# Optimization experiments

Measured on AMD Instinct MI355X. Metric: run time of the kernel, lower is better.

## Reference

```python
import jax, jax.numpy as jnp
import numpy as np

NUM_HEADS = 32      # query heads
NUM_KV_HEADS = 8    # GQA kv heads
HEAD_DIM = 128
BS = 16             # decode batch (one new token per sequence)
KV_LEN = 2048       # pages (page_size=1 -> tokens) per sequence
NUM_SLOTS = BS * KV_LEN
SCALE = HEAD_DIM ** -0.5


def setup_inputs() -> dict:
    key = jax.random.key(0)
    ks = jax.random.split(key, 6)
    q = jax.random.normal(ks[0], (BS, NUM_HEADS * HEAD_DIM), dtype=jnp.float32)
    k = jax.random.normal(ks[1], (BS, NUM_KV_HEADS * HEAD_DIM), dtype=jnp.float32)
    v = jax.random.normal(ks[2], (BS, NUM_KV_HEADS * HEAD_DIM), dtype=jnp.float32)
    k_cache = jax.random.normal(ks[3], (NUM_SLOTS, NUM_KV_HEADS * HEAD_DIM), dtype=jnp.float32)
    v_cache = jax.random.normal(ks[4], (NUM_SLOTS, NUM_KV_HEADS * HEAD_DIM), dtype=jnp.float32)
    # paged layout: each sequence owns KV_LEN non-contiguous slots (page_size=1)
    perm = jax.random.permutation(ks[5], NUM_SLOTS).astype(jnp.int32)
    page_indices = perm.reshape(BS, KV_LEN)            # [BS, KV_LEN] slot ids
    slot_mapping = page_indices[:, -1]                 # new token written to last page
    return {"q": q, "k": k, "v": v, "k_cache": k_cache, "v_cache": v_cache,
            "slot_mapping": slot_mapping, "page_indices": page_indices}


def reference(q, k, v, k_cache, v_cache, slot_mapping, page_indices):
    # store_kvcache: scatter new K/V rows into flat [num_slots, Hkv*d] caches
    k_cache = k_cache.at[slot_mapping].set(k)
    v_cache = v_cache.at[slot_mapping].set(v)
    # paged gather (page_size=1): [BS, KV_LEN, Hkv, d]
    keys = k_cache[page_indices].reshape(BS, KV_LEN, NUM_KV_HEADS, HEAD_DIM)
    vals = v_cache[page_indices].reshape(BS, KV_LEN, NUM_KV_HEADS, HEAD_DIM)
    # GQA: query head h uses kv head h // group
    group = NUM_HEADS // NUM_KV_HEADS
    qh = q.reshape(BS, NUM_KV_HEADS, group, HEAD_DIM)
    scores = jnp.einsum('bhgd,blhd->bhgl', qh, keys) * SCALE   # [BS,Hkv,g,L]
    p = jax.nn.softmax(scores, axis=-1)
    o = jnp.einsum('bhgl,blhd->bhgd', p, vals)                 # [BS,Hkv,g,d]
    return o.reshape(BS, NUM_HEADS * HEAD_DIM)
```

## Files before the change

### kernel.cpp

```cpp
#include <hip/hip_runtime.h>
#include <math.h>

constexpr int NUM_HEADS    = 32;
constexpr int NUM_KV_HEADS = 8;
constexpr int HEAD_DIM     = 128;
constexpr int BS           = 16;
constexpr int KV_LEN       = 2048;
constexpr int GROUP        = NUM_HEADS / NUM_KV_HEADS;
constexpr int NCHUNK       = 16;
constexpr int CHUNK        = KV_LEN / NCHUNK;
constexpr int NIT          = CHUNK / 16;

__global__ __launch_bounds__(256, 4) void attn_partial_kernel(
    const float* __restrict__ q,
    const float* __restrict__ knew,
    const float* __restrict__ vnew,
    const float* __restrict__ k_cache,
    const float* __restrict__ v_cache,
    const int*   __restrict__ page_indices,
    float* __restrict__ ws_o,
    float* __restrict__ ws_m,
    float* __restrict__ ws_s)
{
    const int bid   = blockIdx.x;
    const int chunk = bid % NCHUNK;
    const int h     = (bid / NCHUNK) % NUM_KV_HEADS;
    const int b     = bid / (NCHUNK * NUM_KV_HEADS);

    const int tid  = threadIdx.x;
    const int wid  = tid >> 6;
    const int lane = tid & 63;
    const int g    = lane >> 4;
    const int sub  = lane & 15;
    const int lg   = wid * 4 + g;

    const int lbase = chunk * CHUNK;

    const float qscale = 0.08838834764831845f * 1.4426950408889634f;

    float qv[GROUP][8];
#pragma unroll
    for (int hg = 0; hg < GROUP; ++hg) {
        const float* qp = q + ((size_t)b * NUM_HEADS + h * GROUP + hg) * HEAD_DIM;
        const float4 a = *(const float4*)(qp + sub * 4);
        const float4 c = *(const float4*)(qp + 64 + sub * 4);
        qv[hg][0] = a.x * qscale; qv[hg][1] = a.y * qscale;
        qv[hg][2] = a.z * qscale; qv[hg][3] = a.w * qscale;
        qv[hg][4] = c.x * qscale; qv[hg][5] = c.y * qscale;
        qv[hg][6] = c.z * qscale; qv[hg][7] = c.w * qscale;
    }

    float m[GROUP], ssum[GROUP], o[GROUP][8];
#pragma unroll
    for (int hg = 0; hg < GROUP; ++hg) {
        m[hg] = -INFINITY; ssum[hg] = 0.f;
#pragma unroll
        for (int j = 0; j < 8; ++j) o[hg][j] = 0.f;
    }

    const float* knew_row = knew + ((size_t)b * NUM_KV_HEADS + h) * HEAD_DIM;
    const float* vnew_row = vnew + ((size_t)b * NUM_KV_HEADS + h) * HEAD_DIM;

    int idx_next = page_indices[b * KV_LEN + lbase + lg];

#pragma unroll 1
    for (int it = 0; it < NIT; ++it) {
        const int l   = lbase + it * 16 + lg;
        const int idx = idx_next;
        if (it + 1 < NIT)
            idx_next = page_indices[b * KV_LEN + l + 16];

        const float* kr;
        const float* vr;
        if (l == KV_LEN - 1) {
            kr = knew_row; vr = vnew_row;
        } else {
            kr = k_cache + ((size_t)idx * NUM_KV_HEADS + h) * HEAD_DIM;
            vr = v_cache + ((size_t)idx * NUM_KV_HEADS + h) * HEAD_DIM;
        }
        const float4 k0 = *(const float4*)(kr + sub * 4);
        const float4 k1 = *(const float4*)(kr + 64 + sub * 4);
        const float4 v0 = *(const float4*)(vr + sub * 4);
        const float4 v1 = *(const float4*)(vr + 64 + sub * 4);

        float sc[GROUP];
#pragma unroll
        for (int hg = 0; hg < GROUP; ++hg) {
            sc[hg] = qv[hg][0] * k0.x + qv[hg][1] * k0.y + qv[hg][2] * k0.z + qv[hg][3] * k0.w
                   + qv[hg][4] * k1.x + qv[hg][5] * k1.y + qv[hg][6] * k1.z + qv[hg][7] * k1.w;
        }
#pragma unroll
        for (int off = 1; off < 16; off <<= 1) {
#pragma unroll
            for (int hg = 0; hg < GROUP; ++hg)
                sc[hg] += __shfl_xor(sc[hg], off, 64);
        }
#pragma unroll
        for (int hg = 0; hg < GROUP; ++hg) {
            const float mn = fmaxf(m[hg], sc[hg]);
            const float cf = exp2f(m[hg] - mn);
            const float pr = exp2f(sc[hg] - mn);
            ssum[hg] = ssum[hg] * cf + pr;
            m[hg] = mn;
            o[hg][0] = o[hg][0] * cf + pr * v0.x;
            o[hg][1] = o[hg][1] * cf + pr * v0.y;
            o[hg][2] = o[hg][2] * cf + pr * v0.z;
            o[hg][3] = o[hg][3] * cf + pr * v0.w;
            o[hg][4] = o[hg][4] * cf + pr * v1.x;
            o[hg][5] = o[hg][5] * cf + pr * v1.y;
            o[hg][6] = o[hg][6] * cf + pr * v1.z;
            o[hg][7] = o[hg][7] * cf + pr * v1.w;
        }
    }

#pragma unroll
    for (int off = 16; off <= 32; off <<= 1) {
#pragma unroll
        for (int hg = 0; hg < GROUP; ++hg) {
            const float mo = __shfl_xor(m[hg], off, 64);
            const float so = __shfl_xor(ssum[hg], off, 64);
            float oo[8];
#pragma unroll
            for (int j = 0; j < 8; ++j) oo[j] = __shfl_xor(o[hg][j], off, 64);
            const float mn = fmaxf(m[hg], mo);
            const float c1 = exp2f(m[hg] - mn);
            const float c2 = exp2f(mo - mn);
            ssum[hg] = ssum[hg] * c1 + so * c2;
#pragma unroll
            for (int j = 0; j < 8; ++j) o[hg][j] = o[hg][j] * c1 + oo[j] * c2;
            m[hg] = mn;
        }
    }

    __shared__ float red_o[4][GROUP][HEAD_DIM];
    __shared__ float red_m[4][GROUP];
    __shared__ float red_s[4][GROUP];
    if (lane < 16) {
#pragma unroll
        for (int hg = 0; hg < GROUP; ++hg) {
            *(float4*)&red_o[wid][hg][sub * 4]      = make_float4(o[hg][0], o[hg][1], o[hg][2], o[hg][3]);
            *(float4*)&red_o[wid][hg][64 + sub * 4] = make_float4(o[hg][4], o[hg][5], o[hg][6], o[hg][7]);
        }
        if (sub == 0) {
#pragma unroll
            for (int hg = 0; hg < GROUP; ++hg) { red_m[wid][hg] = m[hg]; red_s[wid][hg] = ssum[hg]; }
        }
    }
    __syncthreads();

    if (wid == 0) {
        const int hg = g;
        const float mn = fmaxf(fmaxf(red_m[0][hg], red_m[1][hg]),
                               fmaxf(red_m[2][hg], red_m[3][hg]));
        float stot = 0.f;
        float acc[8] = {0.f,0.f,0.f,0.f,0.f,0.f,0.f,0.f};
#pragma unroll
        for (int w = 0; w < 4; ++w) {
            const float c = exp2f(red_m[w][hg] - mn);
            stot += red_s[w][hg] * c;
#pragma unroll
            for (int j = 0; j < 4; ++j) acc[j]     += red_o[w][hg][sub * 4 + j] * c;
#pragma unroll
            for (int j = 0; j < 4; ++j) acc[4 + j] += red_o[w][hg][64 + sub * 4 + j] * c;
        }
        const size_t pbase = (((size_t)chunk * BS + b) * NUM_KV_HEADS + h) * GROUP + hg;
        float* op = ws_o + pbase * HEAD_DIM;
        *(float4*)(op + sub * 4)      = make_float4(acc[0], acc[1], acc[2], acc[3]);
        *(float4*)(op + 64 + sub * 4) = make_float4(acc[4], acc[5], acc[6], acc[7]);
        if (sub == 0) { ws_m[pbase] = mn; ws_s[pbase] = stot; }
    }
}

__global__ __launch_bounds__(128) void attn_combine_kernel(
    const float* __restrict__ ws_o,
    const float* __restrict__ ws_m,
    const float* __restrict__ ws_s,
    float* __restrict__ out)
{
    const int bid = blockIdx.x;
    const int hg  = bid % GROUP;
    const int h   = (bid / GROUP) % NUM_KV_HEADS;
    const int b   = bid / (GROUP * NUM_KV_HEADS);
    const int d   = threadIdx.x;

    float mv[NCHUNK];
    float mx = -INFINITY;
#pragma unroll
    for (int c = 0; c < NCHUNK; ++c) {
        mv[c] = ws_m[(((size_t)c * BS + b) * NUM_KV_HEADS + h) * GROUP + hg];
        mx = fmaxf(mx, mv[c]);
    }
    float stot = 0.f, acc = 0.f;
#pragma unroll
    for (int c = 0; c < NCHUNK; ++c) {
        const size_t pbase = (((size_t)c * BS + b) * NUM_KV_HEADS + h) * GROUP + hg;
        const float cf = exp2f(mv[c] - mx);
        stot += ws_s[pbase] * cf;
        acc  += ws_o[pbase * HEAD_DIM + d] * cf;
    }
    out[((size_t)b * NUM_HEADS + h * GROUP + hg) * HEAD_DIM + d] = acc / stot;
}

extern "C" void kernel_launch(void* const* d_in, const int* in_sizes, int n_in,
                              void* d_out, int out_size, void* d_ws, size_t ws_size,
                              hipStream_t stream)
{
    const float* q       = (const float*)d_in[0];
    const float* k       = (const float*)d_in[1];
    const float* v       = (const float*)d_in[2];
    const float* k_cache = (const float*)d_in[3];
    const float* v_cache = (const float*)d_in[4];
    const int* page_indices = (const int*)d_in[6];
    float* out = (float*)d_out;

    float* ws_o = (float*)d_ws;
    float* ws_m = ws_o + (size_t)NCHUNK * BS * NUM_KV_HEADS * GROUP * HEAD_DIM;
    float* ws_s = ws_m + (size_t)NCHUNK * BS * NUM_KV_HEADS * GROUP;

    attn_partial_kernel<<<BS * NUM_KV_HEADS * NCHUNK, 256, 0, stream>>>(
        q, k, v, k_cache, v_cache, page_indices, ws_o, ws_m, ws_s);
    attn_combine_kernel<<<BS * NUM_KV_HEADS * GROUP, 128, 0, stream>>>(
        ws_o, ws_m, ws_s, out);
}
```

Before: 53.72 us.

## Double-buffer paged K/V rows into LDS via async global_load_lds

Each wave now uses global_load_lds DMA to copy its 16 gathered K/V rows into a double-buffered shared-memory region. The next iteration's rows are issued before the current one is consumed from LDS, so the scattered page loads can overlap with the dot-product and softmax work. The reduction scratch now reuses the same shared buffer. In exchange, every iteration needs a block-wide barrier, and correctness depends on the compiler inserting the right wait counts for the async LDS writes.

After: 58.30 us. 1.09x slower.

```diff
diff --git a/kernel.cpp b/kernel.cpp
--- a/kernel.cpp
+++ b/kernel.cpp
@@ -10,6 +10,13 @@
 constexpr int NCHUNK       = 16;
 constexpr int CHUNK        = KV_LEN / NCHUNK;
 constexpr int NIT          = CHUNK / 16;
+
+__device__ __forceinline__ void dma16(const float* g, float* l) {
+    __builtin_amdgcn_global_load_lds(
+        (const __attribute__((address_space(1))) void*)g,
+        (__attribute__((address_space(3))) void*)l,
+        16, 0, 0);
+}
 
 __global__ __launch_bounds__(256, 4) void attn_partial_kernel(
     const float* __restrict__ q,
@@ -36,6 +43,8 @@
 
     const int lbase = chunk * CHUNK;
 
+    __shared__ float smem[2][4][1024];
+
     const float qscale = 0.08838834764831845f * 1.4426950408889634f;
 
     float qv[GROUP][8];
@@ -61,27 +70,40 @@
     const float* knew_row = knew + ((size_t)b * NUM_KV_HEADS + h) * HEAD_DIM;
     const float* vnew_row = vnew + ((size_t)b * NUM_KV_HEADS + h) * HEAD_DIM;
 
-    int idx_next = page_indices[b * KV_LEN + lbase + lg];
-
-#pragma unroll 1
-    for (int it = 0; it < NIT; ++it) {
-        const int l   = lbase + it * 16 + lg;
-        const int idx = idx_next;
-        if (it + 1 < NIT)
-            idx_next = page_indices[b * KV_LEN + l + 16];
-
-        const float* kr;
-        const float* vr;
+    auto stage = [&](int buf, int l, int idx) {
+        const float *kr, *vr;
         if (l == KV_LEN - 1) {
             kr = knew_row; vr = vnew_row;
         } else {
             kr = k_cache + ((size_t)idx * NUM_KV_HEADS + h) * HEAD_DIM;
             vr = v_cache + ((size_t)idx * NUM_KV_HEADS + h) * HEAD_DIM;
         }
-        const float4 k0 = *(const float4*)(kr + sub * 4);
-        const float4 k1 = *(const float4*)(kr + 64 + sub * 4);
-        const float4 v0 = *(const float4*)(vr + sub * 4);
-        const float4 v1 = *(const float4*)(vr + 64 + sub * 4);
+        float* base = &smem[buf][wid][0];
+        dma16(kr + sub * 4,       base);
+        dma16(kr + 64 + sub * 4,  base + 256);
+        dma16(vr + sub * 4,       base + 512);
+        dma16(vr + 64 + sub * 4,  base + 768);
+    };
+
+    int idx_cur = page_indices[b * KV_LEN + lbase + lg];
+    stage(0, lbase + lg, idx_cur);
+    int idx_next = page_indices[b * KV_LEN + lbase + ((NIT > 1) ? 16 : 0) + lg];
+
+#pragma unroll 1
+    for (int t = 0; t < NIT; ++t) {
+        __syncthreads();
+
+        if (t + 1 < NIT) {
+            stage((t + 1) & 1, lbase + (t + 1) * 16 + lg, idx_next);
+            if (t + 2 < NIT)
+                idx_next = page_indices[b * KV_LEN + lbase + (t + 2) * 16 + lg];
+        }
+
+        const float* basep = &smem[t & 1][wid][0];
+        const float4 k0 = *(const float4*)(basep + g * 64 + sub * 4);
+        const float4 k1 = *(const float4*)(basep + 256 + g * 64 + sub * 4);
+        const float4 v0 = *(const float4*)(basep + 512 + g * 64 + sub * 4);
+        const float4 v1 = *(const float4*)(basep + 768 + g * 64 + sub * 4);
 
         float sc[GROUP];
 #pragma unroll
@@ -132,36 +154,44 @@
         }
     }
 
-    __shared__ float red_o[4][GROUP][HEAD_DIM];
-    __shared__ float red_m[4][GROUP];
-    __shared__ float red_s[4][GROUP];
+    __syncthreads();
+    float* red   = &smem[0][0][0];
+    float* red_o = red;
+    float* red_m = red + 2048;
+    float* red_s = red + 2048 + 16;
     if (lane < 16) {
 #pragma unroll
         for (int hg = 0; hg < GROUP; ++hg) {
-            *(float4*)&red_o[wid][hg][sub * 4]      = make_float4(o[hg][0], o[hg][1], o[hg][2], o[hg][3]);
-            *(float4*)&red_o[wid][hg][64 + sub * 4] = make_float4(o[hg][4], o[hg][5], o[hg][6], o[hg][7]);
+            *(float4*)&red_o[(wid * GROUP + hg) * HEAD_DIM + sub * 4] =
+                make_float4(o[hg][0], o[hg][1], o[hg][2], o[hg][3]);
+            *(float4*)&red_o[(wid * GROUP + hg) * HEAD_DIM + 64 + sub * 4] =
+                make_float4(o[hg][4], o[hg][5], o[hg][6], o[hg][7]);
         }
         if (sub == 0) {
 #pragma unroll
-            for (int hg = 0; hg < GROUP; ++hg) { red_m[wid][hg] = m[hg]; red_s[wid][hg] = ssum[hg]; }
+            for (int hg = 0; hg < GROUP; ++hg) {
+                red_m[wid * GROUP + hg] = m[hg];
+                red_s[wid * GROUP + hg] = ssum[hg];
+            }
         }
     }
     __syncthreads();
 
     if (wid == 0) {
         const int hg = g;
-        const float mn = fmaxf(fmaxf(red_m[0][hg], red_m[1][hg]),
-                               fmaxf(red_m[2][hg], red_m[3][hg]));
+        const float mn = fmaxf(fmaxf(red_m[0 * GROUP + hg], red_m[1 * GROUP + hg]),
+                               fmaxf(red_m[2 * GROUP + hg], red_m[3 * GROUP + hg]));
         float stot = 0.f;
         float acc[8] = {0.f,0.f,0.f,0.f,0.f,0.f,0.f,0.f};
 #pragma unroll
         for (int w = 0; w < 4; ++w) {
-            const float c = exp2f(red_m[w][hg] - mn);
-            stot += red_s[w][hg] * c;
-#pragma unroll
-            for (int j = 0; j < 4; ++j) acc[j]     += red_o[w][hg][sub * 4 + j] * c;
-#pragma unroll
-            for (int j = 0; j < 4; ++j) acc[4 + j] += red_o[w][hg][64 + sub * 4 + j] * c;
+            const float c = exp2f(red_m[w * GROUP + hg] - mn);
+            stot += red_s[w * GROUP + hg] * c;
+            const float* ro = &red_o[(w * GROUP + hg) * HEAD_DIM];
+#pragma unroll
+            for (int j = 0; j < 4; ++j) acc[j]     += ro[sub * 4 + j] * c;
+#pragma unroll
+            for (int j = 0; j < 4; ++j) acc[4 + j] += ro[64 + sub * 4 + j] * c;
         }
         const size_t pbase = (((size_t)chunk * BS + b) * NUM_KV_HEADS + h) * GROUP + hg;
         float* op = ws_o + pbase * HEAD_DIM;
```
